# Optimization experiments

Hardware: AMD Instinct MI355X
Metric: run time of the kernel (lower is better)

The kernel has to match this reference:

```python
import jax, jax.numpy as jnp
import numpy as np

N_NODES = 100000
N_EDGES = 1600000
D_IN = 64
D_HID = 64


def setup_inputs() -> dict:
    key = jax.random.key(0)
    k1, k2, k3, k4, k5 = jax.random.split(key, 5)
    features = jax.random.normal(k1, (N_NODES, D_IN), dtype=jnp.float32)
    src = jax.random.randint(k2, (N_EDGES,), 0, N_NODES, dtype=jnp.int64)
    dst = jax.random.randint(k3, (N_EDGES,), 0, N_NODES, dtype=jnp.int64)
    # nn.Linear(in_feats, n_hidden): W is [out, in], b is [out]
    W = jax.random.normal(k4, (D_HID, D_IN), dtype=jnp.float32) * (1.0 / np.sqrt(D_IN))
    b = jax.random.normal(k5, (D_HID,), dtype=jnp.float32) * 0.01
    return {"features": features, "src": src, "dst": dst, "W": W, "b": b}


def reference(features, src, dst, W, b):
    # copy_src + sum: h_agg[v] = sum_{(u->v) in E} features[u]
    msgs = features[src]                                   # [E, D_IN] gather
    h_agg = jax.ops.segment_sum(msgs, dst, num_segments=N_NODES)  # [N, D_IN] scatter-add
    # NodeApplyModule: linear + activation
    h = h_agg @ W.T + b                                    # [N, D_HID]
    return jax.nn.relu(h)
```

## Files before the change

### kernel.cpp

```cpp
#include <hip/hip_runtime.h>
#include <hip/hip_bf16.h>

constexpr int N_NODES = 100000;
constexpr int N_EDGES = 1600000;
constexpr int D = 64;
constexpr int NPB = 64;
constexpr int NBUK = (N_NODES + NPB - 1) / NPB;
constexpr int CAP = 1536;
constexpr int CAP_E = 2304;
constexpr unsigned SENT = 100000u;
constexpr int PART_BLOCKS = 256;
constexpr int CONV_BLOCKS = 64;
constexpr int PREP_THREADS = 1024;
constexpr int EPB = (N_EDGES + PART_BLOCKS - 1) / PART_BLOCKS;

__device__ inline unsigned pack_bf16_2(float a, float b) {
    unsigned ua = __float_as_uint(a), ub = __float_as_uint(b);
    ua = (ua + 0x7FFFu + ((ua >> 16) & 1u)) >> 16;
    ub = (ub + 0x7FFFu + ((ub >> 16) & 1u)) >> 16;
    return ua | (ub << 16);
}

__global__ __launch_bounds__(PREP_THREADS) void prep_kernel(
    const float* __restrict__ feat, const int* __restrict__ src,
    const int* __restrict__ dst, int* __restrict__ gtot,
    unsigned* __restrict__ packed, uint2* __restrict__ fb) {
    const int tid = threadIdx.x;

    if (blockIdx.x >= PART_BLOCKS) {
        const int cb = blockIdx.x - PART_BLOCKS;
        const int total = N_NODES * D / 4;
        const float4* f4 = reinterpret_cast<const float4*>(feat);
        for (int i = cb * PREP_THREADS + tid; i < total; i += CONV_BLOCKS * PREP_THREADS) {
            const float4 v = f4[i];
            fb[i] = make_uint2(pack_bf16_2(v.x, v.y), pack_bf16_2(v.z, v.w));
        }
        if (cb == 0 && tid < 16)
            fb[(size_t)SENT * 16 + tid] = make_uint2(0u, 0u);
        return;
    }

    __shared__ int lcnt[NBUK];
    __shared__ int lbase[NBUK];

    const int lo = blockIdx.x * EPB;
    int hi = lo + EPB; if (hi > N_EDGES) hi = N_EDGES;

    for (int i = tid; i < NBUK; i += PREP_THREADS) lcnt[i] = 0;
    __syncthreads();

    #pragma unroll 4
    for (int e = lo + tid; e < hi; e += PREP_THREADS)
        atomicAdd(&lcnt[dst[e] >> 6], 1);
    __syncthreads();

    for (int i = tid; i < NBUK; i += PREP_THREADS) {
        const int c = lcnt[i];
        lbase[i] = c ? atomicAdd(&gtot[i], c) : 0;
        lcnt[i] = 0;
    }
    __syncthreads();

    #pragma unroll 4
    for (int e = lo + tid; e < hi; e += PREP_THREADS) {
        const int d = dst[e];
        const int buk = d >> 6;
        const int p = lbase[buk] + atomicAdd(&lcnt[buk], 1);
        if (p < CAP)
            packed[(size_t)buk * CAP + p] =
                ((unsigned)(d & (NPB - 1)) << 17) | (unsigned)src[e];
    }
}

__global__ __launch_bounds__(256, 2) void bucket_kernel(
    const uint2* __restrict__ fb, const int* __restrict__ gtot,
    const unsigned* __restrict__ packed, const float* __restrict__ W,
    const float* __restrict__ bias, float* __restrict__ out) {
    __shared__ unsigned elist[CAP_E];
    __shared__ int cnt[NPB];
    __shared__ int cur[NPB];
    __shared__ int pstart[NPB];
    __shared__ float hrow[4][D];

    const int tid = threadIdx.x;
    const int w = tid >> 6;
    const int j = tid & 63;
    const int g = j >> 4;
    const int l = j & 15;
    const int buk = blockIdx.x;

    float4 wr[16];
    #pragma unroll
    for (int q = 0; q < 16; ++q)
        wr[q] = *reinterpret_cast<const float4*>(W + j * D + (q << 2));
    const float bj = bias[j];

    int m = gtot[buk]; if (m > CAP) m = CAP;
    const unsigned* bp = packed + (size_t)buk * CAP;

    if (tid < NPB) cnt[tid] = 0;
    for (int i = tid; i < CAP_E; i += 256) elist[i] = SENT;
    __syncthreads();

    #pragma unroll 4
    for (int i = tid; i < m; i += 256)
        atomicAdd(&cnt[bp[i] >> 17], 1);
    __syncthreads();

    if (tid < 64) {
        const int c = cnt[tid];
        const int pc = (c + 15) & ~15;
        int x = pc;
        #pragma unroll
        for (int o = 1; o < 64; o <<= 1) {
            const int y = __shfl_up(x, o);
            if (tid >= o) x += y;
        }
        pstart[tid] = x - pc;
        cur[tid] = x - pc;
    }
    __syncthreads();

    #pragma unroll 4
    for (int i = tid; i < m; i += 256) {
        const unsigned pk = bp[i];
        const int p = atomicAdd(&cur[pk >> 17], 1);
        elist[p] = pk & 0x1FFFFu;
    }
    __syncthreads();

    const int gbase = buk * NPB;

    for (int n = w; n < NPB; n += 4) {
        const int gn = gbase + n;
        if (gn >= N_NODES) break;
        const int i0 = pstart[n];
        const int e1 = i0 + ((cnt[n] + 15) & ~15);

        float hx = 0.f, hy = 0.f, hz = 0.f, hw_ = 0.f;

        for (int i = i0; i < e1; i += 16) {
            const int s0 = elist[i + g];
            const int s1 = elist[i + 4 + g];
            const int s2 = elist[i + 8 + g];
            const int s3 = elist[i + 12 + g];
            const uint2 q0 = fb[(size_t)s0 * 16 + l];
            const uint2 q1 = fb[(size_t)s1 * 16 + l];
            const uint2 q2 = fb[(size_t)s2 * 16 + l];
            const uint2 q3 = fb[(size_t)s3 * 16 + l];
            hx += __uint_as_float(q0.x << 16) + __uint_as_float(q1.x << 16)
                + __uint_as_float(q2.x << 16) + __uint_as_float(q3.x << 16);
            hy += __uint_as_float(q0.x & 0xFFFF0000u) + __uint_as_float(q1.x & 0xFFFF0000u)
                + __uint_as_float(q2.x & 0xFFFF0000u) + __uint_as_float(q3.x & 0xFFFF0000u);
            hz += __uint_as_float(q0.y << 16) + __uint_as_float(q1.y << 16)
                + __uint_as_float(q2.y << 16) + __uint_as_float(q3.y << 16);
            hw_ += __uint_as_float(q0.y & 0xFFFF0000u) + __uint_as_float(q1.y & 0xFFFF0000u)
                 + __uint_as_float(q2.y & 0xFFFF0000u) + __uint_as_float(q3.y & 0xFFFF0000u);
        }

        hx += __shfl_xor(hx, 16); hx += __shfl_xor(hx, 32);
        hy += __shfl_xor(hy, 16); hy += __shfl_xor(hy, 32);
        hz += __shfl_xor(hz, 16); hz += __shfl_xor(hz, 32);
        hw_ += __shfl_xor(hw_, 16); hw_ += __shfl_xor(hw_, 32);

        if (g == 0)
            *reinterpret_cast<float4*>(&hrow[w][l << 2]) =
                make_float4(hx, hy, hz, hw_);

        float acc = bj;
        #pragma unroll
        for (int q = 0; q < 16; ++q) {
            const float4 hv = *reinterpret_cast<const float4*>(&hrow[w][q << 2]);
            acc = fmaf(hv.x, wr[q].x, acc);
            acc = fmaf(hv.y, wr[q].y, acc);
            acc = fmaf(hv.z, wr[q].z, acc);
            acc = fmaf(hv.w, wr[q].w, acc);
        }
        out[(size_t)gn * D + j] = fmaxf(acc, 0.0f);
    }
}

extern "C" void kernel_launch(void* const* d_in, const int* in_sizes, int n_in,
                              void* d_out, int out_size, void* d_ws, size_t ws_size,
                              hipStream_t stream) {
    const float* feat = (const float*)d_in[0];
    const int*   src  = (const int*)d_in[1];
    const int*   dst  = (const int*)d_in[2];
    const float* W    = (const float*)d_in[3];
    const float* b    = (const float*)d_in[4];
    float* out = (float*)d_out;

    int* gtot = (int*)d_ws;
    unsigned* packed = (unsigned*)((char*)d_ws + 8192);
    uint2* fb = (uint2*)((char*)d_ws + 8192 + (size_t)NBUK * CAP * 4);

    hipMemsetAsync(gtot, 0, NBUK * sizeof(int), stream);

    prep_kernel<<<PART_BLOCKS + CONV_BLOCKS, PREP_THREADS, 0, stream>>>(
        feat, src, dst, gtot, packed, fb);

    bucket_kernel<<<NBUK, 256, 0, stream>>>(fb, gtot, packed, W, b, out);
}
```

Measured before the change: 101.7 us.

## Prefetch next edge chunk across nodes and keep bucket entries in registers

The bucket kernel now loads each thread's packed edge entries (up to six) from global memory once into registers, and uses them for both the counting pass and the scatter pass instead of reading them twice. The gather loop is software-pipelined: each wave owns 16 contiguous nodes and issues the feature loads for the next 16-edge chunk, including the first chunk of the next node, before accumulating the current one. The aim is to hide gather latency and remove the redundant global reads. The cost is more live registers, which may reduce occupancy, and one wasted prefetch at the end of each wave's range.

```diff
diff --git a/kernel.cpp b/kernel.cpp
--- a/kernel.cpp
+++ b/kernel.cpp
@@ -98,13 +98,27 @@
     int m = gtot[buk]; if (m > CAP) m = CAP;
     const unsigned* bp = packed + (size_t)buk * CAP;
 
+    unsigned pk0 = 0, pk1 = 0, pk2 = 0, pk3 = 0, pk4 = 0, pk5 = 0;
+    const bool v0 = tid < m,            v1 = tid + 256 < m;
+    const bool v2 = tid + 512 < m,      v3 = tid + 768 < m;
+    const bool v4 = tid + 1024 < m,     v5 = tid + 1280 < m;
+    if (v0) pk0 = bp[tid];
+    if (v1) pk1 = bp[tid + 256];
+    if (v2) pk2 = bp[tid + 512];
+    if (v3) pk3 = bp[tid + 768];
+    if (v4) pk4 = bp[tid + 1024];
+    if (v5) pk5 = bp[tid + 1280];
+
     if (tid < NPB) cnt[tid] = 0;
     for (int i = tid; i < CAP_E; i += 256) elist[i] = SENT;
     __syncthreads();
 
-    #pragma unroll 4
-    for (int i = tid; i < m; i += 256)
-        atomicAdd(&cnt[bp[i] >> 17], 1);
+    if (v0) atomicAdd(&cnt[pk0 >> 17], 1);
+    if (v1) atomicAdd(&cnt[pk1 >> 17], 1);
+    if (v2) atomicAdd(&cnt[pk2 >> 17], 1);
+    if (v3) atomicAdd(&cnt[pk3 >> 17], 1);
+    if (v4) atomicAdd(&cnt[pk4 >> 17], 1);
+    if (v5) atomicAdd(&cnt[pk5 >> 17], 1);
     __syncthreads();
 
     if (tid < 64) {
@@ -121,33 +135,40 @@
     }
     __syncthreads();
 
-    #pragma unroll 4
-    for (int i = tid; i < m; i += 256) {
-        const unsigned pk = bp[i];
-        const int p = atomicAdd(&cur[pk >> 17], 1);
-        elist[p] = pk & 0x1FFFFu;
-    }
+    if (v0) { const int p = atomicAdd(&cur[pk0 >> 17], 1); elist[p] = pk0 & 0x1FFFFu; }
+    if (v1) { const int p = atomicAdd(&cur[pk1 >> 17], 1); elist[p] = pk1 & 0x1FFFFu; }
+    if (v2) { const int p = atomicAdd(&cur[pk2 >> 17], 1); elist[p] = pk2 & 0x1FFFFu; }
+    if (v3) { const int p = atomicAdd(&cur[pk3 >> 17], 1); elist[p] = pk3 & 0x1FFFFu; }
+    if (v4) { const int p = atomicAdd(&cur[pk4 >> 17], 1); elist[p] = pk4 & 0x1FFFFu; }
+    if (v5) { const int p = atomicAdd(&cur[pk5 >> 17], 1); elist[p] = pk5 & 0x1FFFFu; }
     __syncthreads();
 
     const int gbase = buk * NPB;
-
-    for (int n = w; n < NPB; n += 4) {
-        const int gn = gbase + n;
-        if (gn >= N_NODES) break;
-        const int i0 = pstart[n];
-        const int e1 = i0 + ((cnt[n] + 15) & ~15);
+    const int n0 = w << 4;
+
+    int pf = pstart[n0];
+    uint2 q0 = fb[(size_t)elist[pf + g] * 16 + l];
+    uint2 q1 = fb[(size_t)elist[pf + 4 + g] * 16 + l];
+    uint2 q2 = fb[(size_t)elist[pf + 8 + g] * 16 + l];
+    uint2 q3 = fb[(size_t)elist[pf + 12 + g] * 16 + l];
+
+    for (int n = n0; n < n0 + 16; ++n) {
+        int i = pstart[n];
+        const int e1 = i + ((cnt[n] + 15) & ~15);
+        const int nextstart = (n + 1 < NPB) ? pstart[n + 1] : 0;
 
         float hx = 0.f, hy = 0.f, hz = 0.f, hw_ = 0.f;
 
-        for (int i = i0; i < e1; i += 16) {
-            const int s0 = elist[i + g];
-            const int s1 = elist[i + 4 + g];
-            const int s2 = elist[i + 8 + g];
-            const int s3 = elist[i + 12 + g];
-            const uint2 q0 = fb[(size_t)s0 * 16 + l];
-            const uint2 q1 = fb[(size_t)s1 * 16 + l];
-            const uint2 q2 = fb[(size_t)s2 * 16 + l];
-            const uint2 q3 = fb[(size_t)s3 * 16 + l];
+        while (i < e1) {
+            const int i_nxt = (i + 16 < e1) ? (i + 16) : nextstart;
+            const int t0 = elist[i_nxt + g];
+            const int t1 = elist[i_nxt + 4 + g];
+            const int t2 = elist[i_nxt + 8 + g];
+            const int t3 = elist[i_nxt + 12 + g];
+            const uint2 r0 = fb[(size_t)t0 * 16 + l];
+            const uint2 r1 = fb[(size_t)t1 * 16 + l];
+            const uint2 r2 = fb[(size_t)t2 * 16 + l];
+            const uint2 r3 = fb[(size_t)t3 * 16 + l];
             hx += __uint_as_float(q0.x << 16) + __uint_as_float(q1.x << 16)
                 + __uint_as_float(q2.x << 16) + __uint_as_float(q3.x << 16);
             hy += __uint_as_float(q0.x & 0xFFFF0000u) + __uint_as_float(q1.x & 0xFFFF0000u)
@@ -156,6 +177,8 @@
                 + __uint_as_float(q2.y << 16) + __uint_as_float(q3.y << 16);
             hw_ += __uint_as_float(q0.y & 0xFFFF0000u) + __uint_as_float(q1.y & 0xFFFF0000u)
                  + __uint_as_float(q2.y & 0xFFFF0000u) + __uint_as_float(q3.y & 0xFFFF0000u);
+            q0 = r0; q1 = r1; q2 = r2; q3 = r3;
+            i += 16;
         }
 
         hx += __shfl_xor(hx, 16); hx += __shfl_xor(hx, 32);
@@ -176,7 +199,8 @@
             acc = fmaf(hv.z, wr[q].z, acc);
             acc = fmaf(hv.w, wr[q].w, acc);
         }
-        out[(size_t)gn * D + j] = fmaxf(acc, 0.0f);
+        const int gn = gbase + n;
+        if (gn < N_NODES) out[(size_t)gn * D + j] = fmaxf(acc, 0.0f);
     }
 }
 
```

Result: no change. 102.0 us (+0.2%).
